# Kernel optimization log

Measured on AMD Instinct MI355X. Metric: run time of the kernel, lower is better.

The kernel has to match this reference:

```python
import jax, jax.numpy as jnp
import numpy as np

TEMP = 0.5  # init temperature
EPS = 1e-12  # F.normalize eps


def setup_inputs() -> dict:
    key = jax.random.key(0)
    k1, k2 = jax.random.split(key)
    batch_embedding = jax.random.normal(k1, (4096, 256), dtype=jnp.float32)
    labels = jax.random.randint(k2, (4096,), 0, 512, dtype=jnp.int64)
    return {"batch_embedding": batch_embedding, "labels": labels}


def reference(batch_embedding, labels):
    n = labels.shape[0]
    dt = batch_embedding.dtype
    # row-normalize; cosine_similarity of normalized rows == norm @ norm.T
    nrm = jnp.linalg.norm(batch_embedding, axis=1, keepdims=True)
    norm = batch_embedding / jnp.maximum(nrm, EPS)
    sim = norm @ norm.T  # [n, n]
    mask = (labels[:, None] == labels[None, :]).astype(dt)  # same-label pairs (incl. diagonal)
    eye = jnp.eye(n, dtype=dt)
    exp_sim = jnp.exp(sim / TEMP) * (1.0 - eye)  # zero diagonal
    pos = mask * exp_sim
    neg_sum = jnp.sum(exp_sim - pos, axis=1)  # per-row negative sum
    ratio = pos / (pos + neg_sum[:, None])
    loss_mat = -jnp.log((1.0 - mask) + ratio + eye)
    nnz = jnp.count_nonzero(loss_mat).astype(dt)
    return jnp.sum(loss_mat) / nnz
```

## Files before the change

kernel.cpp:

```cpp
#include <hip/hip_runtime.h>
#include <hip/hip_bf16.h>


#define N_ROWS 4096
#define K_DIM  256

typedef __attribute__((ext_vector_type(4))) float float4v;
typedef __attribute__((ext_vector_type(4))) float f4;
typedef __attribute__((ext_vector_type(4))) int   int4v;
typedef __attribute__((ext_vector_type(2))) long  long2v;

#define PK_OFF    0
#define PART_OFF  (2 * 1024 * 1024)
#define ACC_OFF   (PART_OFF + 4 * 64 * N_ROWS * 4)

__device__ __forceinline__ void gll16(const void* g, void* l) {
    __builtin_amdgcn_global_load_lds(
        (const __attribute__((address_space(1))) unsigned int*)g,
        (__attribute__((address_space(3))) unsigned int*)l, 16, 0, 0);
}

__global__ void normalize_kernel(const float* __restrict__ emb,
                                 unsigned char* __restrict__ pk8,
                                 float* __restrict__ acc) {
    int tile = blockIdx.x, t = threadIdx.x;
    __shared__ float lds[16 * 256];
    __shared__ float sc[16];
    const f4* src = (const f4*)(emb + tile * 16 * 256);
    f4* dst4 = (f4*)lds;
    #pragma unroll
    for (int it = 0; it < 4; ++it) dst4[t + 256 * it] = src[t + 256 * it];
    __syncthreads();
    int wave = t >> 6, lane = t & 63;
    int row = wave * 4 + (lane >> 4);
    float s = 0.f;
    #pragma unroll
    for (int m = 0; m < 16; ++m) {
        float x = lds[row * 256 + (lane & 15) + 16 * m];
        s += x * x;
    }
    s += __shfl_xor(s, 1); s += __shfl_xor(s, 2);
    s += __shfl_xor(s, 4); s += __shfl_xor(s, 8);
    float scale = 1.0f / fmaxf(sqrtf(s), 1e-12f);
    if ((lane & 15) == 0) sc[row] = scale;
    __syncthreads();
    int u = t >> 6, quad = (t >> 4) & 3, r16 = t & 15;
    float s8 = sc[r16] * 8.0f;
    const float* lr = lds + r16 * 256;
    int4v wv;
    #pragma unroll
    for (int wi = 0; wi < 4; ++wi) {
        int h  = wi >> 1;
        int j0 = (wi & 1) * 4;
        int kb = quad * 8 + (2 * u + h) * 32 + j0;
        float v0 = lr[kb + 0] * s8, v1 = lr[kb + 1] * s8;
        float v2 = lr[kb + 2] * s8, v3 = lr[kb + 3] * s8;
        int wd = __builtin_amdgcn_cvt_pk_fp8_f32(v0, v1, 0, 0);
        wd     = __builtin_amdgcn_cvt_pk_fp8_f32(v2, v3, wd, 1);
        wv[wi] = wd;
    }
    *(int4v*)(pk8 + tile * 4096 + t * 16) = wv;
    if (tile == 0 && t < 4) acc[t] = 0.0f;
}

__global__ __launch_bounds__(256, 3)
void negsum_kernel(const unsigned char* __restrict__ pk8,
                   const int* __restrict__ labels,
                   float* __restrict__ part) {
    __shared__ __align__(16) unsigned char Bs8[32768];
    int t = threadIdx.x;
    int w = t >> 6, lane = t & 63;
    int lane16 = lane & 15, quad = lane >> 4;
    int xcd = blockIdx.x & 7, local = blockIdx.x >> 3;
    int bi = xcd * 4 + (local >> 5);
    int bj = local & 31;
    int wi = w >> 1, wj = w & 1;

    int ibase = bi * 128 + wi * 64;
    int jbase = bj * 128 + wj * 64;
    const char* pkb = (const char*)pk8;

    #pragma unroll
    for (int u = 0; u < 8; ++u) {
        int c8 = w * 8 + u, tl = c8 >> 2, cs = c8 & 3;
        gll16(pkb + (((bj * 8 + tl) << 12) | (cs << 10)) + lane * 16,
              Bs8 + (c8 << 10));
    }
    long2v av[4][4];
    #pragma unroll
    for (int it = 0; it < 4; ++it)
        #pragma unroll
        for (int cs = 0; cs < 4; ++cs)
            av[it][cs] = *(const long2v*)(pkb
                + (((bi * 8 + wi * 4 + it) << 12) | (cs << 10)) + lane * 16);

    int labi[16], labj[4];
    #pragma unroll
    for (int it = 0; it < 4; ++it)
        #pragma unroll
        for (int r = 0; r < 4; ++r)
            labi[it * 4 + r] = labels[ibase + it * 16 + quad * 4 + r];
    #pragma unroll
    for (int jt = 0; jt < 4; ++jt)
        labj[jt] = labels[jbase + jt * 16 + lane16];

    float4v acc[4][4];
    #pragma unroll
    for (int a = 0; a < 4; ++a)
        #pragma unroll
        for (int b = 0; b < 4; ++b)
            acc[a][b] = (float4v){0.f, 0.f, 0.f, 0.f};

    __syncthreads();

    #pragma unroll
    for (int cs = 0; cs < 4; ++cs) {
        long2v bv[4];
        #pragma unroll
        for (int jt = 0; jt < 4; ++jt)
            bv[jt] = *(const long2v*)(Bs8
                     + (((((wj * 4 + jt) << 2) | cs) << 10)) + lane * 16);
        #pragma unroll
        for (int h = 0; h < 2; ++h)
            #pragma unroll
            for (int it = 0; it < 4; ++it)
                #pragma unroll
                for (int jt = 0; jt < 4; ++jt)
                    acc[it][jt] = __builtin_amdgcn_mfma_f32_16x16x32_fp8_fp8(
                        av[it][cs][h], bv[jt][h], acc[it][jt], 0, 0, 0);
    }

    float ex[4] = {0,0,0,0}, pe[4] = {0,0,0,0};
    float tt[4] = {0,0,0,0}, pc[4] = {0,0,0,0};
    #pragma unroll
    for (int it = 0; it < 4; ++it) {
        #pragma unroll
        for (int jt = 0; jt < 4; ++jt) {
            int j = jbase + jt * 16 + lane16;
            #pragma unroll
            for (int r = 0; r < 4; ++r) {
                int i = ibase + it * 16 + quad * 4 + r;
                float t2 = acc[it][jt][r] * 0.03125f;
                float e  = __expf(t2);
                bool keep = (i != j);
                bool same = (labi[it * 4 + r] == labj[jt]);
                ex[jt] += keep ? e : 0.0f;
                float m = (same && keep) ? 1.0f : 0.0f;
                pe[jt] = fmaf(m, e,  pe[jt]);
                tt[jt] = fmaf(m, t2, tt[jt]);
                pc[jt] += m;
            }
        }
    }
    int i64 = bi * 2 + wi;
    #pragma unroll
    for (int jt = 0; jt < 4; ++jt) {
        float v0 = ex[jt], v1 = pe[jt], v2 = tt[jt], v3 = pc[jt];
        v0 += __shfl_xor(v0, 16); v0 += __shfl_xor(v0, 32);
        v1 += __shfl_xor(v1, 16); v1 += __shfl_xor(v1, 32);
        v2 += __shfl_xor(v2, 16); v2 += __shfl_xor(v2, 32);
        v3 += __shfl_xor(v3, 16); v3 += __shfl_xor(v3, 32);
        if (quad == 0) {
            int col = jbase + jt * 16 + lane16;
            part[((0 * 64 + i64) << 12) + col] = v0;
            part[((1 * 64 + i64) << 12) + col] = v1;
            part[((2 * 64 + i64) << 12) + col] = v2;
            part[((3 * 64 + i64) << 12) + col] = v3;
        }
    }
}

__global__ void rowreduce_kernel(const float* __restrict__ part,
                                 float* __restrict__ acc,
                                 float* __restrict__ out) {
    int t = threadIdx.x;
    int rl = t >> 3, sl = t & 7;
    int row = blockIdx.x * 32 + rl;
    float s[4];
    #pragma unroll
    for (int st = 0; st < 4; ++st) {
        float v = 0.f;
        #pragma unroll
        for (int c = 0; c < 8; ++c)
            v += part[((st * 64 + (sl * 8 + c)) << 12) + row];
        s[st] = v;
    }
    #pragma unroll
    for (int st = 0; st < 4; ++st) {
        s[st] += __shfl_xor(s[st], 1);
        s[st] += __shfl_xor(s[st], 2);
        s[st] += __shfl_xor(s[st], 4);
    }
    float lsum = 0.f, pcm = 0.f;
    if (sl == 0 && s[3] > 0.f) {
        float n = s[0] - s[1];
        lsum = s[3] * logf(n) + s[1] / n - s[2];
        pcm  = s[3];
    }
    #pragma unroll
    for (int m = 1; m < 64; m <<= 1) {
        lsum += __shfl_xor(lsum, m);
        pcm  += __shfl_xor(pcm,  m);
    }
    __shared__ float sl4[4], sc4[4];
    int wave = t >> 6, lane = t & 63;
    if (lane == 0) { sl4[wave] = lsum; sc4[wave] = pcm; }
    __syncthreads();
    if (t == 0) {
        atomicAdd(&acc[0], sl4[0] + sl4[1] + sl4[2] + sl4[3]);
        atomicAdd(&acc[1], sc4[0] + sc4[1] + sc4[2] + sc4[3]);
        __threadfence();
        int ticket = atomicAdd((int*)(acc + 2), 1);
        if (ticket == 127) {
            float ls = atomicAdd(&acc[0], 0.0f);
            float cs = atomicAdd(&acc[1], 0.0f);
            out[0] = ls / cs;
        }
    }
}

extern "C" void kernel_launch(void* const* d_in, const int* in_sizes, int n_in,
                              void* d_out, int out_size, void* d_ws, size_t ws_size,
                              hipStream_t stream) {
    const float* emb    = (const float*)d_in[0];
    const int*   labels = (const int*)d_in[1];
    float* out = (float*)d_out;
    char*  ws  = (char*)d_ws;

    unsigned char* pk8  = (unsigned char*)(ws + PK_OFF);
    float*         part = (float*)(ws + PART_OFF);
    float*         acc  = (float*)(ws + ACC_OFF);

    normalize_kernel<<<N_ROWS / 16, 256, 0, stream>>>(emb, pk8, acc);
    negsum_kernel<<<1024, 256, 0, stream>>>(pk8, labels, part);
    rowreduce_kernel<<<128, 256, 0, stream>>>(part, acc, out);
}
```

Baseline: 79.34 us.

## Fuse row reduction into negsum kernel via atomic column stats and last-block finish

Removes the separate rowreduce kernel and the large per-tile partials buffer. Each negsum block first combines its two wave-row halves in LDS, then atomically adds four per-column statistics into a small 4x4096 buffer. A ticket counter picks the last block, which computes the final loss. This saves a kernel launch and the partials traffic, but adds global float atomics (contention on columns shared across 32 row blocks) and a serial final reduction in a single block.

```diff
diff --git a/kernel.cpp b/kernel.cpp
--- a/kernel.cpp
+++ b/kernel.cpp
@@ -11,8 +11,8 @@
 typedef __attribute__((ext_vector_type(2))) long  long2v;
 
 #define PK_OFF    0
-#define PART_OFF  (2 * 1024 * 1024)
-#define ACC_OFF   (PART_OFF + 4 * 64 * N_ROWS * 4)
+#define CS_OFF    (2 * 1024 * 1024)
+#define ACC_OFF   (CS_OFF + 4 * N_ROWS * 4)
 
 __device__ __forceinline__ void gll16(const void* g, void* l) {
     __builtin_amdgcn_global_load_lds(
@@ -22,6 +22,7 @@
 
 __global__ void normalize_kernel(const float* __restrict__ emb,
                                  unsigned char* __restrict__ pk8,
+                                 float* __restrict__ colstats,
                                  float* __restrict__ acc) {
     int tile = blockIdx.x, t = threadIdx.x;
     __shared__ float lds[16 * 256];
@@ -60,14 +61,20 @@
         wv[wi] = wd;
     }
     *(int4v*)(pk8 + tile * 4096 + t * 16) = wv;
+    if (t < 16) ((f4*)colstats)[tile * 16 + t] = (f4){0.f, 0.f, 0.f, 0.f};
     if (tile == 0 && t < 4) acc[t] = 0.0f;
 }
 
 __global__ __launch_bounds__(256, 3)
 void negsum_kernel(const unsigned char* __restrict__ pk8,
                    const int* __restrict__ labels,
-                   float* __restrict__ part) {
+                   float* __restrict__ colstats,
+                   float* __restrict__ acc,
+                   float* __restrict__ out) {
     __shared__ __align__(16) unsigned char Bs8[32768];
+    __shared__ float red[2][4][64];
+    __shared__ int   lastf;
+    __shared__ float fin[8];
     int t = threadIdx.x;
     int w = t >> 6, lane = t & 63;
     int lane16 = lane & 15, quad = lane >> 4;
@@ -104,12 +111,12 @@
     for (int jt = 0; jt < 4; ++jt)
         labj[jt] = labels[jbase + jt * 16 + lane16];
 
-    float4v acc[4][4];
+    float4v acc4[4][4];
     #pragma unroll
     for (int a = 0; a < 4; ++a)
         #pragma unroll
         for (int b = 0; b < 4; ++b)
-            acc[a][b] = (float4v){0.f, 0.f, 0.f, 0.f};
+            acc4[a][b] = (float4v){0.f, 0.f, 0.f, 0.f};
 
     __syncthreads();
 
@@ -126,8 +133,8 @@
             for (int it = 0; it < 4; ++it)
                 #pragma unroll
                 for (int jt = 0; jt < 4; ++jt)
-                    acc[it][jt] = __builtin_amdgcn_mfma_f32_16x16x32_fp8_fp8(
-                        av[it][cs][h], bv[jt][h], acc[it][jt], 0, 0, 0);
+                    acc4[it][jt] = __builtin_amdgcn_mfma_f32_16x16x32_fp8_fp8(
+                        av[it][cs][h], bv[jt][h], acc4[it][jt], 0, 0, 0);
     }
 
     float ex[4] = {0,0,0,0}, pe[4] = {0,0,0,0};
@@ -140,7 +147,7 @@
             #pragma unroll
             for (int r = 0; r < 4; ++r) {
                 int i = ibase + it * 16 + quad * 4 + r;
-                float t2 = acc[it][jt][r] * 0.03125f;
+                float t2 = acc4[it][jt][r] * 0.03125f;
                 float e  = __expf(t2);
                 bool keep = (i != j);
                 bool same = (labi[it * 4 + r] == labj[jt]);
@@ -152,7 +159,7 @@
             }
         }
     }
-    int i64 = bi * 2 + wi;
+    float vs[4];
     #pragma unroll
     for (int jt = 0; jt < 4; ++jt) {
         float v0 = ex[jt], v1 = pe[jt], v2 = tt[jt], v3 = pc[jt];
@@ -160,62 +167,56 @@
         v1 += __shfl_xor(v1, 16); v1 += __shfl_xor(v1, 32);
         v2 += __shfl_xor(v2, 16); v2 += __shfl_xor(v2, 32);
         v3 += __shfl_xor(v3, 16); v3 += __shfl_xor(v3, 32);
-        if (quad == 0) {
+        float vsel = (quad == 0) ? v0 : (quad == 1) ? v1
+                   : (quad == 2) ? v2 : v3;
+        vs[jt] = vsel;
+        if (wi == 0) red[wj][quad][jt * 16 + lane16] = vsel;
+    }
+    __syncthreads();
+    if (wi == 1) {
+        #pragma unroll
+        for (int jt = 0; jt < 4; ++jt) {
             int col = jbase + jt * 16 + lane16;
-            part[((0 * 64 + i64) << 12) + col] = v0;
-            part[((1 * 64 + i64) << 12) + col] = v1;
-            part[((2 * 64 + i64) << 12) + col] = v2;
-            part[((3 * 64 + i64) << 12) + col] = v3;
-        }
-    }
-}
-
-__global__ void rowreduce_kernel(const float* __restrict__ part,
-                                 float* __restrict__ acc,
-                                 float* __restrict__ out) {
-    int t = threadIdx.x;
-    int rl = t >> 3, sl = t & 7;
-    int row = blockIdx.x * 32 + rl;
-    float s[4];
-    #pragma unroll
-    for (int st = 0; st < 4; ++st) {
-        float v = 0.f;
-        #pragma unroll
-        for (int c = 0; c < 8; ++c)
-            v += part[((st * 64 + (sl * 8 + c)) << 12) + row];
-        s[st] = v;
-    }
-    #pragma unroll
-    for (int st = 0; st < 4; ++st) {
-        s[st] += __shfl_xor(s[st], 1);
-        s[st] += __shfl_xor(s[st], 2);
-        s[st] += __shfl_xor(s[st], 4);
-    }
-    float lsum = 0.f, pcm = 0.f;
-    if (sl == 0 && s[3] > 0.f) {
-        float n = s[0] - s[1];
-        lsum = s[3] * logf(n) + s[1] / n - s[2];
-        pcm  = s[3];
-    }
-    #pragma unroll
-    for (int m = 1; m < 64; m <<= 1) {
-        lsum += __shfl_xor(lsum, m);
-        pcm  += __shfl_xor(pcm,  m);
-    }
-    __shared__ float sl4[4], sc4[4];
-    int wave = t >> 6, lane = t & 63;
-    if (lane == 0) { sl4[wave] = lsum; sc4[wave] = pcm; }
+            atomicAdd(colstats + (quad << 12) + col,
+                      vs[jt] + red[wj][quad][jt * 16 + lane16]);
+        }
+    }
+    __threadfence();
     __syncthreads();
     if (t == 0) {
-        atomicAdd(&acc[0], sl4[0] + sl4[1] + sl4[2] + sl4[3]);
-        atomicAdd(&acc[1], sc4[0] + sc4[1] + sc4[2] + sc4[3]);
-        __threadfence();
-        int ticket = atomicAdd((int*)(acc + 2), 1);
-        if (ticket == 127) {
-            float ls = atomicAdd(&acc[0], 0.0f);
-            float cs = atomicAdd(&acc[1], 0.0f);
-            out[0] = ls / cs;
-        }
+        int tk = atomicAdd((int*)(acc + 2), 1);
+        lastf = (tk == 1023) ? 1 : 0;
+    }
+    __syncthreads();
+    if (lastf) {
+        float lsum = 0.f, csum = 0.f;
+        #pragma unroll
+        for (int c = 0; c < 16; ++c) {
+            int col = (c << 8) + t;
+            float exs = __hip_atomic_load(colstats + col,
+                            __ATOMIC_RELAXED, __HIP_MEMORY_SCOPE_AGENT);
+            float pes = __hip_atomic_load(colstats + 4096 + col,
+                            __ATOMIC_RELAXED, __HIP_MEMORY_SCOPE_AGENT);
+            float tts = __hip_atomic_load(colstats + 2 * 4096 + col,
+                            __ATOMIC_RELAXED, __HIP_MEMORY_SCOPE_AGENT);
+            float pcs = __hip_atomic_load(colstats + 3 * 4096 + col,
+                            __ATOMIC_RELAXED, __HIP_MEMORY_SCOPE_AGENT);
+            if (pcs > 0.f) {
+                float n = exs - pes;
+                lsum += pcs * logf(n) + pes / n - tts;
+                csum += pcs;
+            }
+        }
+        #pragma unroll
+        for (int m = 1; m < 64; m <<= 1) {
+            lsum += __shfl_xor(lsum, m);
+            csum += __shfl_xor(csum, m);
+        }
+        if (lane == 0) { fin[w] = lsum; fin[4 + w] = csum; }
+        __syncthreads();
+        if (t == 0)
+            out[0] = (fin[0] + fin[1] + fin[2] + fin[3]) /
+                     (fin[4] + fin[5] + fin[6] + fin[7]);
     }
 }
 
@@ -227,11 +228,10 @@
     float* out = (float*)d_out;
     char*  ws  = (char*)d_ws;
 
-    unsigned char* pk8  = (unsigned char*)(ws + PK_OFF);
-    float*         part = (float*)(ws + PART_OFF);
-    float*         acc  = (float*)(ws + ACC_OFF);
-
-    normalize_kernel<<<N_ROWS / 16, 256, 0, stream>>>(emb, pk8, acc);
-    negsum_kernel<<<1024, 256, 0, stream>>>(pk8, labels, part);
-    rowreduce_kernel<<<128, 256, 0, stream>>>(part, acc, out);
-}
+    unsigned char* pk8      = (unsigned char*)(ws + PK_OFF);
+    float*         colstats = (float*)(ws + CS_OFF);
+    float*         acc      = (float*)(ws + ACC_OFF);
+
+    normalize_kernel<<<N_ROWS / 16, 256, 0, stream>>>(emb, pk8, colstats, acc);
+    negsum_kernel<<<1024, 256, 0, stream>>>(pk8, labels, colstats, acc, out);
+}
```

Result: slower. 133.9 us (+68.7%).

## Exploit Gram-matrix symmetry: compute upper-triangular tiles and emit transposed partials

Applied to the files above, without the earlier changes.

The similarity matrix is symmetric, so the negsum kernel now launches only the 528 upper-triangular 128x128 tiles instead of all 1024. Each off-diagonal tile also reduces its results along rows to write the per-column partial sums for the mirrored tile. This roughly halves the FP8 MFMA work, at the cost of a second exp/reduction epilogue per off-diagonal tile, a serial loop to decode the tile index, and loss of the previous XCD-aware block mapping.

```diff
diff --git a/kernel.cpp b/kernel.cpp
--- a/kernel.cpp
+++ b/kernel.cpp
@@ -71,9 +71,9 @@
     int t = threadIdx.x;
     int w = t >> 6, lane = t & 63;
     int lane16 = lane & 15, quad = lane >> 4;
-    int xcd = blockIdx.x & 7, local = blockIdx.x >> 3;
-    int bi = xcd * 4 + (local >> 5);
-    int bj = local & 31;
+    int bi = 0, rem = blockIdx.x;
+    while (rem >= 32 - bi) { rem -= 32 - bi; ++bi; }
+    int bj = bi + rem;
     int wi = w >> 1, wj = w & 1;
 
     int ibase = bi * 128 + wi * 64;
@@ -168,6 +168,53 @@
             part[((3 * 64 + i64) << 12) + col] = v3;
         }
     }
+
+    if (bi != bj) {
+        int j64 = bj * 2 + wj;
+        #pragma unroll
+        for (int it = 0; it < 4; ++it) {
+            float rex[4] = {0,0,0,0}, rpe[4] = {0,0,0,0};
+            float rtt[4] = {0,0,0,0}, rpc[4] = {0,0,0,0};
+            #pragma unroll
+            for (int jt = 0; jt < 4; ++jt) {
+                bool same0 = (labi[it * 4 + 0] == labj[jt]);
+                bool same1 = (labi[it * 4 + 1] == labj[jt]);
+                bool same2 = (labi[it * 4 + 2] == labj[jt]);
+                bool same3 = (labi[it * 4 + 3] == labj[jt]);
+                #pragma unroll
+                for (int r = 0; r < 4; ++r) {
+                    float t2 = acc[it][jt][r] * 0.03125f;
+                    float e  = __expf(t2);
+                    bool same = (r == 0) ? same0 : (r == 1) ? same1
+                              : (r == 2) ? same2 : same3;
+                    float m = same ? 1.0f : 0.0f;
+                    rex[r] += e;
+                    rpe[r] = fmaf(m, e,  rpe[r]);
+                    rtt[r] = fmaf(m, t2, rtt[r]);
+                    rpc[r] += m;
+                }
+            }
+            #pragma unroll
+            for (int r = 0; r < 4; ++r) {
+                float v0 = rex[r], v1 = rpe[r], v2 = rtt[r], v3 = rpc[r];
+                v0 += __shfl_xor(v0, 1); v0 += __shfl_xor(v0, 2);
+                v0 += __shfl_xor(v0, 4); v0 += __shfl_xor(v0, 8);
+                v1 += __shfl_xor(v1, 1); v1 += __shfl_xor(v1, 2);
+                v1 += __shfl_xor(v1, 4); v1 += __shfl_xor(v1, 8);
+                v2 += __shfl_xor(v2, 1); v2 += __shfl_xor(v2, 2);
+                v2 += __shfl_xor(v2, 4); v2 += __shfl_xor(v2, 8);
+                v3 += __shfl_xor(v3, 1); v3 += __shfl_xor(v3, 2);
+                v3 += __shfl_xor(v3, 4); v3 += __shfl_xor(v3, 8);
+                if (lane16 == 0) {
+                    int i = ibase + it * 16 + quad * 4 + r;
+                    part[((0 * 64 + j64) << 12) + i] = v0;
+                    part[((1 * 64 + j64) << 12) + i] = v1;
+                    part[((2 * 64 + j64) << 12) + i] = v2;
+                    part[((3 * 64 + j64) << 12) + i] = v3;
+                }
+            }
+        }
+    }
 }
 
 __global__ void rowreduce_kernel(const float* __restrict__ part,
@@ -232,6 +279,6 @@
     float*         acc  = (float*)(ws + ACC_OFF);
 
     normalize_kernel<<<N_ROWS / 16, 256, 0, stream>>>(emb, pk8, acc);
-    negsum_kernel<<<1024, 256, 0, stream>>>(pk8, labels, part);
+    negsum_kernel<<<528, 256, 0, stream>>>(pk8, labels, part);
     rowreduce_kernel<<<128, 256, 0, stream>>>(part, acc, out);
 }
```

Result: slower. 95.30 us (+20.1%).
